# Optimization experiments

Measured on AMD Instinct MI355X. Metric: run time of the kernel, lower is better.

The kernel has to match this reference:

```python
import jax, jax.numpy as jnp
import numpy as np

B, N, IN, HID, OUT = 32768, 16, 64, 128, 128

def setup_inputs() -> dict:
    key = jax.random.key(0)
    ks = jax.random.split(key, 8)
    x = jax.random.normal(ks[0], (B * N, IN), dtype=jnp.float32)
    edge_index0 = jax.random.randint(ks[1], (B * 8,), 0, B * N, dtype=jnp.int64)
    adj_param = jnp.ones((N, N), dtype=jnp.float32)
    s1 = 1.0 / np.sqrt(IN)
    s2 = 1.0 / np.sqrt(HID)
    W_rel1 = jax.random.normal(ks[2], (IN, HID), dtype=jnp.float32) * s1
    b_rel1 = jax.random.normal(ks[3], (HID,), dtype=jnp.float32) * s1
    W_root1 = jax.random.normal(ks[4], (IN, HID), dtype=jnp.float32) * s1
    W_rel2 = jax.random.normal(ks[5], (HID, OUT), dtype=jnp.float32) * s2
    b_rel2 = jax.random.normal(ks[6], (OUT,), dtype=jnp.float32) * s2
    W_root2 = jax.random.normal(ks[7], (HID, OUT), dtype=jnp.float32) * s2
    return {"x": x, "edge_index0": edge_index0, "adj_param": adj_param,
            "W_rel1": W_rel1, "b_rel1": b_rel1, "W_root1": W_root1,
            "W_rel2": W_rel2, "b_rel2": b_rel2, "W_root2": W_root2}

def _dense_sage(x, adj, W_rel, b_rel, W_root):
    # DenseSAGEConv: mean-aggregate neighbors via dense adj, then lin_rel + lin_root
    agg = jnp.einsum('bij,bjf->bif', adj, x)                     # [B,N,F]
    deg = jnp.maximum(adj.sum(-1, keepdims=True), 1.0)           # clamp(min=1)
    return (agg / deg) @ W_rel + b_rel + x @ W_root

def reference(x, edge_index0, adj_param, W_rel1, b_rel1, W_root1, W_rel2, b_rel2, W_root2):
    b = x.shape[0] // N
    xb = x.reshape(b, N, -1)
    # nodes touched by an edge keep adjacency; others masked out (rows and cols zeroed)
    mask = jnp.ones((b * N,), dtype=bool).at[edge_index0].set(False).reshape(b, N)
    drop = mask[:, :, None] | mask[:, None, :]                   # [B,N,N]
    adj = jnp.where(drop, 0.0, adj_param[None, :, :])
    h = jax.nn.relu(_dense_sage(xb, adj, W_rel1, b_rel1, W_root1))
    out = _dense_sage(h, adj, W_rel2, b_rel2, W_root2)
    return out.reshape(b * N, -1)
```

## Files before the change

### kernel.cpp

```cpp
#include <hip/hip_runtime.h>

typedef unsigned short u16;
typedef float floatx4 __attribute__((ext_vector_type(4)));
typedef short shortx8 __attribute__((ext_vector_type(8)));

#define MFMA16(a, b, c) __builtin_amdgcn_mfma_f32_16x16x32_bf16(a, b, c, 0, 0, 0)

__device__ __forceinline__ u16 f2b(float f) {
    union { float f; unsigned u; } c;
    c.f = f;
    unsigned lsb = (c.u >> 16) & 1u;
    c.u += 0x7fffu + lsb;
    return (u16)(c.u >> 16);
}

__global__ __launch_bounds__(256) void scatter_flags(const int* __restrict__ e,
                                                     unsigned char* __restrict__ fl,
                                                     int n) {
    int i = blockIdx.x * 256 + threadIdx.x;
    if (i < n) fl[e[i]] = 1;
}

__global__ __launch_bounds__(256) void prep_weights(
    const float* __restrict__ W1r, const float* __restrict__ W1o,
    const float* __restrict__ W2r, const float* __restrict__ W2o,
    u16* __restrict__ W1rt, u16* __restrict__ W1ot,
    u16* __restrict__ W2rt, u16* __restrict__ W2ot)
{
    int t = blockIdx.x * 256 + threadIdx.x;
    union { u16 h[4]; unsigned long long ll; } pk;
    if (t < 2048) {
        int n = t >> 4, k0 = (t & 15) * 4;
        #pragma unroll
        for (int j = 0; j < 4; ++j) pk.h[j] = f2b(W1r[(k0 + j) * 128 + n]);
        *(unsigned long long*)(W1rt + n * 64 + k0) = pk.ll;
    } else if (t < 4096) {
        int tt = t - 2048; int n = tt >> 4, k0 = (tt & 15) * 4;
        #pragma unroll
        for (int j = 0; j < 4; ++j) pk.h[j] = f2b(W1o[(k0 + j) * 128 + n]);
        *(unsigned long long*)(W1ot + n * 64 + k0) = pk.ll;
    } else if (t < 8192) {
        int tt = t - 4096; int n = tt >> 5, k0 = (tt & 31) * 4;
        #pragma unroll
        for (int j = 0; j < 4; ++j) pk.h[j] = f2b(W2r[(k0 + j) * 128 + n]);
        *(unsigned long long*)(W2rt + n * 128 + k0) = pk.ll;
    } else if (t < 12288) {
        int tt = t - 8192; int n = tt >> 5, k0 = (tt & 31) * 4;
        #pragma unroll
        for (int j = 0; j < 4; ++j) pk.h[j] = f2b(W2o[(k0 + j) * 128 + n]);
        *(unsigned long long*)(W2ot + n * 128 + k0) = pk.ll;
    }
}

__global__ __launch_bounds__(256, 3) void sage_mfma(
    const float* __restrict__ x,
    const unsigned char* __restrict__ flags,
    const float* __restrict__ adjp,
    const float* __restrict__ br1,
    const float* __restrict__ br2,
    const u16* __restrict__ W1rt,
    const u16* __restrict__ W1ot,
    const u16* __restrict__ W2rt,
    const u16* __restrict__ W2ot,
    float* __restrict__ out)
{
    __shared__ __align__(16) unsigned char smem[44544];
    u16*   s_w    = (u16*)smem;
    float* s_flag = (float*)(smem + 4096);
    float* s_inv  = (float*)(smem + 4352);
    u16*   s_t    = (u16*)(smem + 4608);
    u16*   s_x    = (u16*)(smem + 27136);
    u16*   s_h    = (u16*)(smem + 27136);

    const int b   = blockIdx.x;
    const int tid = threadIdx.x;
    const int w   = tid >> 6;
    const int l   = tid & 63;
    const int q   = l >> 4;
    const int lr  = l & 15;
    const int tn0 = 2 * w;
    const floatx4 fz = {0.f, 0.f, 0.f, 0.f};

    {
        uint4 z = {0, 0, 0, 0};
        uint4* tz = (uint4*)s_t;
        #pragma unroll
        for (int i = 0; i < 6; ++i) { int idx = tid + i * 256; if (idx < 1408) tz[idx] = z; }
    }
    if (tid < 64) s_flag[tid] = flags[b * 64 + tid] ? 1.0f : 0.0f;
    {
        const float4* xg = (const float4*)(x + (size_t)b * 4096);
        #pragma unroll
        for (int i = 0; i < 4; ++i) {
            int e = tid + i * 256;
            float4 v = xg[e];
            int row = e >> 4, f = (e & 15) * 4;
            union { u16 h[4]; unsigned long long ll; } pk;
            pk.h[0] = f2b(v.x); pk.h[1] = f2b(v.y); pk.h[2] = f2b(v.z); pk.h[3] = f2b(v.w);
            *(unsigned long long*)(s_x + row * 72 + f) = pk.ll;
        }
    }
    __syncthreads();
    if (tid < 64) {
        int g = tid >> 4, i = tid & 15;
        float s = 0.f;
        #pragma unroll
        for (int j = 0; j < 16; ++j) s += adjp[i * 16 + j] * s_flag[g * 16 + j];
        s *= s_flag[tid];
        s_inv[tid] = 1.0f / fmaxf(s, 1.0f);
    }
    __syncthreads();
    {
        int flat = tid * 8;
        int g = flat >> 9, rem = flat & 511, i = rem >> 5, k0 = rem & 31;
        float ti = s_flag[g * 16 + i] * s_inv[g * 16 + i];
        union { u16 h[8]; uint4 v; } pk;
        #pragma unroll
        for (int j = 0; j < 8; ++j) {
            int k = k0 + j;
            float val = (k < 16) ? ti * s_flag[g * 16 + k] * adjp[i * 16 + k] : 0.f;
            pk.h[j] = f2b(val);
        }
        *(uint4*)(s_w + g * 512 + i * 32 + k0) = pk.v;
    }
    shortx8 b1r[2][2], b1o[2][2];
    float bias1[2], bias2[2];
    #pragma unroll
    for (int tni = 0; tni < 2; ++tni) {
        int n = (tn0 + tni) * 16 + lr;
        bias1[tni] = br1[n]; bias2[tni] = br2[n];
        #pragma unroll
        for (int ks = 0; ks < 2; ++ks) {
            b1r[tni][ks] = *(const shortx8*)(W1rt + n * 64 + ks * 32 + q * 8);
            b1o[tni][ks] = *(const shortx8*)(W1ot + n * 64 + ks * 32 + q * 8);
        }
    }
    __syncthreads();

    floatx4 y2acc[4][2];
    #pragma unroll
    for (int tm = 0; tm < 4; ++tm) {
        shortx8 ax[2];
        #pragma unroll
        for (int ks = 0; ks < 2; ++ks)
            ax[ks] = *(const shortx8*)(s_x + (tm * 16 + lr) * 72 + ks * 32 + q * 8);
        floatx4 y1[2] = {fz, fz};
        #pragma unroll
        for (int tni = 0; tni < 2; ++tni) {
            y2acc[tm][tni] = fz;
            #pragma unroll
            for (int ks = 0; ks < 2; ++ks) {
                y1[tni]        = MFMA16(ax[ks], b1r[tni][ks], y1[tni]);
                y2acc[tm][tni] = MFMA16(ax[ks], b1o[tni][ks], y2acc[tm][tni]);
            }
        }
        #pragma unroll
        for (int tni = 0; tni < 2; ++tni) {
            union { u16 h[4]; unsigned long long ll; } pk;
            #pragma unroll
            for (int r = 0; r < 4; ++r) pk.h[r] = f2b(y1[tni][r]);
            *(unsigned long long*)(s_t + ((tn0 + tni) * 16 + lr) * 88 + tm * 16 + q * 4) = pk.ll;
        }
    }
    __syncthreads();

    shortx8 wfrag[4];
    #pragma unroll
    for (int g = 0; g < 4; ++g)
        wfrag[g] = *(const shortx8*)(s_w + g * 512 + lr * 32 + q * 8);
    #pragma unroll
    for (int g = 0; g < 4; ++g) {
        #pragma unroll
        for (int tni = 0; tni < 2; ++tni) {
            shortx8 bf = *(const shortx8*)(s_t + ((tn0 + tni) * 16 + lr) * 88 + g * 16 + q * 8);
            floatx4 a = MFMA16(wfrag[g], bf, fz);
            #pragma unroll
            for (int r = 0; r < 4; ++r) {
                float hv = fmaxf(a[r] + y2acc[g][tni][r] + bias1[tni], 0.f);
                s_h[(g * 16 + q * 4 + r) * 136 + (tn0 + tni) * 16 + lr] = f2b(hv);
            }
        }
    }
    __syncthreads();

    shortx8 b2r[2][4], b2o[2][4];
    #pragma unroll
    for (int tni = 0; tni < 2; ++tni) {
        int n = (tn0 + tni) * 16 + lr;
        #pragma unroll
        for (int ks = 0; ks < 4; ++ks) {
            b2r[tni][ks] = *(const shortx8*)(W2rt + n * 128 + ks * 32 + q * 8);
            b2o[tni][ks] = *(const shortx8*)(W2ot + n * 128 + ks * 32 + q * 8);
        }
    }
    floatx4 u2acc[4][2];
    #pragma unroll
    for (int tm = 0; tm < 4; ++tm) {
        shortx8 ah[4];
        #pragma unroll
        for (int ks = 0; ks < 4; ++ks)
            ah[ks] = *(const shortx8*)(s_h + (tm * 16 + lr) * 136 + ks * 32 + q * 8);
        floatx4 u1[2] = {fz, fz};
        #pragma unroll
        for (int tni = 0; tni < 2; ++tni) {
            u2acc[tm][tni] = fz;
            #pragma unroll
            for (int ks = 0; ks < 4; ++ks) {
                u1[tni]        = MFMA16(ah[ks], b2r[tni][ks], u1[tni]);
                u2acc[tm][tni] = MFMA16(ah[ks], b2o[tni][ks], u2acc[tm][tni]);
            }
        }
        #pragma unroll
        for (int tni = 0; tni < 2; ++tni) {
            union { u16 h[4]; unsigned long long ll; } pk;
            #pragma unroll
            for (int r = 0; r < 4; ++r) pk.h[r] = f2b(u1[tni][r]);
            *(unsigned long long*)(s_t + ((tn0 + tni) * 16 + lr) * 88 + tm * 16 + q * 4) = pk.ll;
        }
    }
    __syncthreads();

    #pragma unroll
    for (int g = 0; g < 4; ++g) {
        #pragma unroll
        for (int tni = 0; tni < 2; ++tni) {
            shortx8 bf = *(const shortx8*)(s_t + ((tn0 + tni) * 16 + lr) * 88 + g * 16 + q * 8);
            floatx4 a = MFMA16(wfrag[g], bf, fz);
            float* op = out + ((size_t)b * 64 + g * 16 + q * 4) * 128 + (tn0 + tni) * 16 + lr;
            #pragma unroll
            for (int r = 0; r < 4; ++r)
                op[r * 128] = a[r] + u2acc[g][tni][r] + bias2[tni];
        }
    }
}

extern "C" void kernel_launch(void* const* d_in, const int* in_sizes, int n_in,
                              void* d_out, int out_size, void* d_ws, size_t ws_size,
                              hipStream_t stream) {
    const float* x    = (const float*)d_in[0];
    const int*   edge = (const int*)d_in[1];
    const float* adjp = (const float*)d_in[2];
    const float* W1r  = (const float*)d_in[3];
    const float* br1  = (const float*)d_in[4];
    const float* W1o  = (const float*)d_in[5];
    const float* W2r  = (const float*)d_in[6];
    const float* br2  = (const float*)d_in[7];
    const float* W2o  = (const float*)d_in[8];
    float* out = (float*)d_out;

    const int total_nodes = in_sizes[0] / 64;
    const int nedge       = in_sizes[1];
    const int nblocks     = total_nodes / 64;

    unsigned char* flags = (unsigned char*)d_ws;
    u16* wbase = (u16*)((char*)d_ws + 524288);
    u16* W1rt = wbase;
    u16* W1ot = wbase + 8192;
    u16* W2rt = wbase + 16384;
    u16* W2ot = wbase + 32768;

    hipMemsetAsync(flags, 0, (size_t)total_nodes, stream);
    scatter_flags<<<(nedge + 255) / 256, 256, 0, stream>>>(edge, flags, nedge);
    prep_weights<<<48, 256, 0, stream>>>(W1r, W1o, W2r, W2o, W1rt, W1ot, W2rt, W2ot);
    sage_mfma<<<nblocks, 256, 0, stream>>>(x, flags, adjp, br1, br2,
                                           W1rt, W1ot, W2rt, W2ot, out);
}
```

Baseline: 451.2 us.

## Fuse adjacency aggregation into register MFMA chain, dropping staging buffer

Builds the normalized adjacency fragment in registers per wave and applies it straight to the transposed per-tile product through a second MFMA, so the s_t staging buffer, its zeroing and two barriers go away. The root-path MFMA is computed transposed with the bias preloaded as its accumulator, which lets the final output be written as contiguous float4 rows. Shared memory drops from about 44 KB to 28 KB and launch bounds rise to 5 blocks per CU for occupancy. The extra MFMA feeds half-zero operands, adding issued MFMA work, and register pressure under the tighter bound could spill.

```diff
diff --git a/kernel.cpp b/kernel.cpp
--- a/kernel.cpp
+++ b/kernel.cpp
@@ -52,7 +52,7 @@
     }
 }
 
-__global__ __launch_bounds__(256, 3) void sage_mfma(
+__global__ __launch_bounds__(256, 5) void sage_mfma(
     const float* __restrict__ x,
     const unsigned char* __restrict__ flags,
     const float* __restrict__ adjp,
@@ -64,13 +64,11 @@
     const u16* __restrict__ W2ot,
     float* __restrict__ out)
 {
-    __shared__ __align__(16) unsigned char smem[44544];
-    u16*   s_w    = (u16*)smem;
-    float* s_flag = (float*)(smem + 4096);
-    float* s_inv  = (float*)(smem + 4352);
-    u16*   s_t    = (u16*)(smem + 4608);
-    u16*   s_x    = (u16*)(smem + 27136);
-    u16*   s_h    = (u16*)(smem + 27136);
+    __shared__ __align__(16) unsigned char smem[27904];
+    u16*   s_x   = (u16*)smem;
+    u16*   s_h   = (u16*)(smem + 9216);
+    float* s_adj = (float*)(smem + 26624);
+    float* s_flag= (float*)(smem + 27648);
 
     const int b   = blockIdx.x;
     const int tid = threadIdx.x;
@@ -82,13 +80,6 @@
     const floatx4 fz = {0.f, 0.f, 0.f, 0.f};
 
     {
-        uint4 z = {0, 0, 0, 0};
-        uint4* tz = (uint4*)s_t;
-        #pragma unroll
-        for (int i = 0; i < 6; ++i) { int idx = tid + i * 256; if (idx < 1408) tz[idx] = z; }
-    }
-    if (tid < 64) s_flag[tid] = flags[b * 64 + tid] ? 1.0f : 0.0f;
-    {
         const float4* xg = (const float4*)(x + (size_t)b * 4096);
         #pragma unroll
         for (int i = 0; i < 4; ++i) {
@@ -100,136 +91,91 @@
             *(unsigned long long*)(s_x + row * 72 + f) = pk.ll;
         }
     }
+    if (tid < 64) s_flag[tid] = flags[b * 64 + tid] ? 1.0f : 0.0f;
+    s_adj[tid] = adjp[tid];
     __syncthreads();
-    if (tid < 64) {
-        int g = tid >> 4, i = tid & 15;
+
+    shortx8 wb8[4];
+    #pragma unroll
+    for (int g = 0; g < 4; ++g) {
         float s = 0.f;
         #pragma unroll
-        for (int j = 0; j < 16; ++j) s += adjp[i * 16 + j] * s_flag[g * 16 + j];
-        s *= s_flag[tid];
-        s_inv[tid] = 1.0f / fmaxf(s, 1.0f);
-    }
-    __syncthreads();
-    {
-        int flat = tid * 8;
-        int g = flat >> 9, rem = flat & 511, i = rem >> 5, k0 = rem & 31;
-        float ti = s_flag[g * 16 + i] * s_inv[g * 16 + i];
-        union { u16 h[8]; uint4 v; } pk;
-        #pragma unroll
-        for (int j = 0; j < 8; ++j) {
-            int k = k0 + j;
-            float val = (k < 16) ? ti * s_flag[g * 16 + k] * adjp[i * 16 + k] : 0.f;
-            pk.h[j] = f2b(val);
-        }
-        *(uint4*)(s_w + g * 512 + i * 32 + k0) = pk.v;
-    }
+        for (int j = 0; j < 16; ++j) s += s_adj[lr * 16 + j] * s_flag[g * 16 + j];
+        float fi = s_flag[g * 16 + lr];
+        float ti = fi / fmaxf(s * fi, 1.0f);
+        #pragma unroll
+        for (int jj = 0; jj < 4; ++jj) {
+            int j = q * 4 + jj;
+            wb8[g][jj] = (short)f2b(ti * s_flag[g * 16 + j] * s_adj[lr * 16 + j]);
+            wb8[g][jj + 4] = 0;
+        }
+    }
+
     shortx8 b1r[2][2], b1o[2][2];
-    float bias1[2], bias2[2];
+    floatx4 bias1[2], bias2[2];
     #pragma unroll
     for (int tni = 0; tni < 2; ++tni) {
-        int n = (tn0 + tni) * 16 + lr;
-        bias1[tni] = br1[n]; bias2[tni] = br2[n];
+        int n0 = (tn0 + tni) * 16;
+        bias1[tni] = *(const floatx4*)(br1 + n0 + q * 4);
+        bias2[tni] = *(const floatx4*)(br2 + n0 + q * 4);
+        int n = n0 + lr;
         #pragma unroll
         for (int ks = 0; ks < 2; ++ks) {
             b1r[tni][ks] = *(const shortx8*)(W1rt + n * 64 + ks * 32 + q * 8);
             b1o[tni][ks] = *(const shortx8*)(W1ot + n * 64 + ks * 32 + q * 8);
         }
     }
-    __syncthreads();
-
-    floatx4 y2acc[4][2];
+
     #pragma unroll
     for (int tm = 0; tm < 4; ++tm) {
         shortx8 ax[2];
         #pragma unroll
         for (int ks = 0; ks < 2; ++ks)
             ax[ks] = *(const shortx8*)(s_x + (tm * 16 + lr) * 72 + ks * 32 + q * 8);
-        floatx4 y1[2] = {fz, fz};
         #pragma unroll
         for (int tni = 0; tni < 2; ++tni) {
-            y2acc[tm][tni] = fz;
+            floatx4 y1 = fz, y2t = bias1[tni];
             #pragma unroll
             for (int ks = 0; ks < 2; ++ks) {
-                y1[tni]        = MFMA16(ax[ks], b1r[tni][ks], y1[tni]);
-                y2acc[tm][tni] = MFMA16(ax[ks], b1o[tni][ks], y2acc[tm][tni]);
+                y1  = MFMA16(ax[ks], b1r[tni][ks], y1);
+                y2t = MFMA16(b1o[tni][ks], ax[ks], y2t);
             }
-        }
-        #pragma unroll
-        for (int tni = 0; tni < 2; ++tni) {
+            shortx8 a1 = {(short)f2b(y1[0]), (short)f2b(y1[1]),
+                          (short)f2b(y1[2]), (short)f2b(y1[3]), 0, 0, 0, 0};
+            floatx4 ag = MFMA16(a1, wb8[tm], y2t);
             union { u16 h[4]; unsigned long long ll; } pk;
             #pragma unroll
-            for (int r = 0; r < 4; ++r) pk.h[r] = f2b(y1[tni][r]);
-            *(unsigned long long*)(s_t + ((tn0 + tni) * 16 + lr) * 88 + tm * 16 + q * 4) = pk.ll;
+            for (int r = 0; r < 4; ++r) pk.h[r] = f2b(fmaxf(ag[r], 0.f));
+            *(unsigned long long*)(s_h + (tm * 16 + lr) * 136 +
+                                   (tn0 + tni) * 16 + q * 4) = pk.ll;
         }
     }
     __syncthreads();
 
-    shortx8 wfrag[4];
-    #pragma unroll
-    for (int g = 0; g < 4; ++g)
-        wfrag[g] = *(const shortx8*)(s_w + g * 512 + lr * 32 + q * 8);
-    #pragma unroll
-    for (int g = 0; g < 4; ++g) {
-        #pragma unroll
-        for (int tni = 0; tni < 2; ++tni) {
-            shortx8 bf = *(const shortx8*)(s_t + ((tn0 + tni) * 16 + lr) * 88 + g * 16 + q * 8);
-            floatx4 a = MFMA16(wfrag[g], bf, fz);
-            #pragma unroll
-            for (int r = 0; r < 4; ++r) {
-                float hv = fmaxf(a[r] + y2acc[g][tni][r] + bias1[tni], 0.f);
-                s_h[(g * 16 + q * 4 + r) * 136 + (tn0 + tni) * 16 + lr] = f2b(hv);
-            }
-        }
-    }
-    __syncthreads();
-
-    shortx8 b2r[2][4], b2o[2][4];
     #pragma unroll
     for (int tni = 0; tni < 2; ++tni) {
         int n = (tn0 + tni) * 16 + lr;
+        shortx8 b2r[4], b2o[4];
         #pragma unroll
         for (int ks = 0; ks < 4; ++ks) {
-            b2r[tni][ks] = *(const shortx8*)(W2rt + n * 128 + ks * 32 + q * 8);
-            b2o[tni][ks] = *(const shortx8*)(W2ot + n * 128 + ks * 32 + q * 8);
-        }
-    }
-    floatx4 u2acc[4][2];
-    #pragma unroll
-    for (int tm = 0; tm < 4; ++tm) {
-        shortx8 ah[4];
-        #pragma unroll
-        for (int ks = 0; ks < 4; ++ks)
-            ah[ks] = *(const shortx8*)(s_h + (tm * 16 + lr) * 136 + ks * 32 + q * 8);
-        floatx4 u1[2] = {fz, fz};
-        #pragma unroll
-        for (int tni = 0; tni < 2; ++tni) {
-            u2acc[tm][tni] = fz;
+            b2r[ks] = *(const shortx8*)(W2rt + n * 128 + ks * 32 + q * 8);
+            b2o[ks] = *(const shortx8*)(W2ot + n * 128 + ks * 32 + q * 8);
+        }
+        #pragma unroll
+        for (int tm = 0; tm < 4; ++tm) {
+            floatx4 u1 = fz, u2t = bias2[tni];
             #pragma unroll
             for (int ks = 0; ks < 4; ++ks) {
-                u1[tni]        = MFMA16(ah[ks], b2r[tni][ks], u1[tni]);
-                u2acc[tm][tni] = MFMA16(ah[ks], b2o[tni][ks], u2acc[tm][tni]);
+                shortx8 ah = *(const shortx8*)(s_h + (tm * 16 + lr) * 136 +
+                                               ks * 32 + q * 8);
+                u1  = MFMA16(ah, b2r[ks], u1);
+                u2t = MFMA16(b2o[ks], ah, u2t);
             }
-        }
-        #pragma unroll
-        for (int tni = 0; tni < 2; ++tni) {
-            union { u16 h[4]; unsigned long long ll; } pk;
-            #pragma unroll
-            for (int r = 0; r < 4; ++r) pk.h[r] = f2b(u1[tni][r]);
-            *(unsigned long long*)(s_t + ((tn0 + tni) * 16 + lr) * 88 + tm * 16 + q * 4) = pk.ll;
-        }
-    }
-    __syncthreads();
-
-    #pragma unroll
-    for (int g = 0; g < 4; ++g) {
-        #pragma unroll
-        for (int tni = 0; tni < 2; ++tni) {
-            shortx8 bf = *(const shortx8*)(s_t + ((tn0 + tni) * 16 + lr) * 88 + g * 16 + q * 8);
-            floatx4 a = MFMA16(wfrag[g], bf, fz);
-            float* op = out + ((size_t)b * 64 + g * 16 + q * 4) * 128 + (tn0 + tni) * 16 + lr;
-            #pragma unroll
-            for (int r = 0; r < 4; ++r)
-                op[r * 128] = a[r] + u2acc[g][tni][r] + bias2[tni];
+            shortx8 a2 = {(short)f2b(u1[0]), (short)f2b(u1[1]),
+                          (short)f2b(u1[2]), (short)f2b(u1[3]), 0, 0, 0, 0};
+            floatx4 og = MFMA16(a2, wb8[tm], u2t);
+            *(floatx4*)(out + ((size_t)b * 64 + tm * 16 + lr) * 128 +
+                        (tn0 + tni) * 16 + q * 4) = og;
         }
     }
 }
```

Measured after the change: 458.6 us. Within noise of the previous version (+1.6%).
